# Performance work log

Hardware: AMD Instinct MI355X
Metric: run time of the kernel (lower is better)

## Reference

```python
import jax, jax.numpy as jnp
import numpy as np

# QLoRA NF4 levels (sorted), standard 16-value normal-float-4 codebook
NF4_LEVELS = jnp.array([
    -1.0, -0.6961928009986877, -0.5250730514526367, -0.39491748809814453,
    -0.28444138169288635, -0.18477343022823334, -0.09105003625154495, 0.0,
    0.07958029955625534, 0.16093020141124725, 0.24611230194568634,
    0.33791524171829224, 0.44070982933044434, 0.5626170039176941,
    0.8481764793395996, 1.0], dtype=jnp.float32)
NF4_MIDPOINTS = (NF4_LEVELS[1:] + NF4_LEVELS[:-1]) * 0.5  # nearest-level boundaries

BLOCK_SIZE = 64
SIGMA_FACTOR = 3.0
EPS = 1e-12


def fake_quantize_tcfp12(x, block_size=BLOCK_SIZE, nf4_residual=True,
                         nf_aware_scaling=True, sigma_factor=SIGMA_FACTOR):
    """Block-wise TCFP-12 fake quantize: int8 main component (nf-aware scale)
    + NF4-quantized residual. Returns dequantized tensor, same shape as x."""
    shape = x.shape
    xb = x.reshape(-1, block_size)                      # [N, B]
    absmax = jnp.max(jnp.abs(xb), axis=1, keepdims=True)
    if nf_aware_scaling:
        std = jnp.std(xb, axis=1, keepdims=True)
        scale = jnp.minimum(absmax, sigma_factor * std)
    else:
        scale = absmax
    scale = jnp.maximum(scale, EPS)
    # 8-bit symmetric main quantize (values beyond scale are clipped)
    q = jnp.clip(jnp.round(xb / scale * 127.0), -127.0, 127.0)
    main = q * (scale / 127.0)
    # 4-bit NF4 residual
    res = xb - main
    if nf4_residual:
        rmax = jnp.maximum(jnp.max(jnp.abs(res), axis=1, keepdims=True), EPS)
        rn = res / rmax                                  # normalized to [-1, 1]
        idx = jnp.searchsorted(NF4_MIDPOINTS, rn)        # nearest NF4 level
        rq = NF4_LEVELS[idx] * rmax
    else:
        rmax = jnp.maximum(jnp.max(jnp.abs(res), axis=1, keepdims=True), EPS)
        rq = jnp.clip(jnp.round(res / rmax * 7.0), -7.0, 7.0) * (rmax / 7.0)
    return (main + rq).reshape(shape)


def ste_fake_quantize(x):
    # straight-through estimator: forward quantizes, backward is identity
    return x + jax.lax.stop_gradient(fake_quantize_tcfp12(x) - x)


def setup_inputs() -> dict:
    key = jax.random.key(0)
    k1, k2 = jax.random.split(key)
    num_embeddings, embedding_dim = 50257, 768
    batch, seq = 8, 4096
    indices = jax.random.randint(k1, (batch, seq), 0, num_embeddings, dtype=jnp.int64 if jax.config.jax_enable_x64 else jnp.int32)
    weight = jax.random.normal(k2, (num_embeddings, embedding_dim), dtype=jnp.float32)
    weight = weight.at[0].set(0.0)  # padding_idx = 0
    return {"indices": indices, "weight": weight}


def reference(indices, weight):
    raw = weight[indices]            # [batch, seq, embedding_dim] gather
    return ste_fake_quantize(raw)
```

## Files before the change

### kernel.cpp

```cpp
#include <hip/hip_runtime.h>
#include <cstddef>


typedef float fx4 __attribute__((ext_vector_type(4)));
typedef int   ix2 __attribute__((ext_vector_type(2)));

namespace {

constexpr float kL[16] = {
    -1.0f, -0.6961928009986877f, -0.5250730514526367f, -0.39491748809814453f,
    -0.28444138169288635f, -0.18477343022823334f, -0.09105003625154495f, 0.0f,
    0.07958029955625534f, 0.16093020141124725f, 0.24611230194568634f,
    0.33791524171829224f, 0.44070982933044434f, 0.5626170039176941f,
    0.8481764793395996f, 1.0f};

}

__device__ __constant__ float kNF4Levels[16] = {
    -1.0f, -0.6961928009986877f, -0.5250730514526367f, -0.39491748809814453f,
    -0.28444138169288635f, -0.18477343022823334f, -0.09105003625154495f, 0.0f,
    0.07958029955625534f, 0.16093020141124725f, 0.24611230194568634f,
    0.33791524171829224f, 0.44070982933044434f, 0.5626170039176941f,
    0.8481764793395996f, 1.0f};

template <int CTRL>
__device__ __forceinline__ float dpp_rorf(float v) {
  return __builtin_bit_cast(
      float, __builtin_amdgcn_update_dpp(0, __builtin_bit_cast(int, v), CTRL,
                                         0xF, 0xF, true));
}

__device__ __forceinline__ fx4 tcfp12_quantize(fx4 x, const ix2* bins) {
  float am = fmaxf(fmaxf(fabsf(x.x), fabsf(x.y)), fmaxf(fabsf(x.z), fabsf(x.w)));
  float s  = (x.x + x.y) + (x.z + x.w);
  float ss = fmaf(x.x, x.x, fmaf(x.y, x.y, fmaf(x.z, x.z, x.w * x.w)));
  am = fmaxf(am, dpp_rorf<0x121>(am)); s += dpp_rorf<0x121>(s); ss += dpp_rorf<0x121>(ss);
  am = fmaxf(am, dpp_rorf<0x122>(am)); s += dpp_rorf<0x122>(s); ss += dpp_rorf<0x122>(ss);
  am = fmaxf(am, dpp_rorf<0x124>(am)); s += dpp_rorf<0x124>(s); ss += dpp_rorf<0x124>(ss);
  am = fmaxf(am, dpp_rorf<0x128>(am)); s += dpp_rorf<0x128>(s); ss += dpp_rorf<0x128>(ss);

  const float mean  = s * 0.015625f;
  const float var   = fmaxf(ss * 0.015625f - mean * mean, 0.0f);
  const float scale = fmaxf(fminf(am, 3.0f * sqrtf(var)), 1e-12f);
  const float to_q   = 127.0f / scale;
  const float from_q = scale / 127.0f;

  const float q0 = __builtin_amdgcn_fmed3f(rintf(x.x * to_q), -127.0f, 127.0f);
  const float q1 = __builtin_amdgcn_fmed3f(rintf(x.y * to_q), -127.0f, 127.0f);
  const float q2 = __builtin_amdgcn_fmed3f(rintf(x.z * to_q), -127.0f, 127.0f);
  const float q3 = __builtin_amdgcn_fmed3f(rintf(x.w * to_q), -127.0f, 127.0f);
  const float m0 = q0 * from_q, m1 = q1 * from_q, m2 = q2 * from_q, m3 = q3 * from_q;
  const float r0 = x.x - m0, r1 = x.y - m1, r2 = x.z - m2, r3 = x.w - m3;

  float rm = fmaxf(fmaxf(fabsf(r0), fabsf(r1)), fmaxf(fabsf(r2), fabsf(r3)));
  rm = fmaxf(rm, dpp_rorf<0x121>(rm));
  rm = fmaxf(rm, dpp_rorf<0x122>(rm));
  rm = fmaxf(rm, dpp_rorf<0x124>(rm));
  rm = fmaxf(rm, dpp_rorf<0x128>(rm));
  rm = fmaxf(rm, 1e-12f);
  const float invr = 1.0f / rm;
  const float rmq  = rm * (1.0f / 127.0f);

  fx4 o;
#pragma unroll
  for (int e = 0; e < 4; ++e) {
    const float r  = (e == 0) ? r0 : (e == 1) ? r1 : (e == 2) ? r2 : r3;
    const float mn = (e == 0) ? m0 : (e == 1) ? m1 : (e == 2) ? m2 : m3;
    const float rn = r * invr;
    const float t  = fmaf(rn, 32.0f, 32.0f);
    int j = (int)t;
    j = (j > 63) ? 63 : j;
    const ix2 b = bins[j];
    const float mstar = __builtin_bit_cast(float, b.x);
    const int   off   = (rn > mstar) ? 8 : 0;
    const int   li    = (int)((signed char)((b.y >> off) & 0xff));
    const float oe = fmaf((float)li, rmq, mn);
    if (e == 0) o.x = oe; else if (e == 1) o.y = oe;
    else if (e == 2) o.z = oe; else o.w = oe;
  }
  return o;
}

__global__ void __launch_bounds__(192)
tcfp_embedding_kernel(const int* __restrict__ indices,
                      const float* __restrict__ weight,
                      float* __restrict__ out,
                      int dim, int nrows) {
  __shared__ ix2 bins[64];
  const int tid = threadIdx.x;
  if (tid < 64) {
    const int j = tid;
    const float L = j * 0.03125f - 1.0f;
    int base = 0;
#pragma unroll
    for (int k = 0; k < 15; ++k) {
      const float mid = (kL[k] + kL[k + 1]) * 0.5f;
      base += (mid < L) ? 1 : 0;
    }
    float mstar = 2.0f;
    float lo = kNF4Levels[base];
    float hi = lo;
    if (base < 15) {
      float mb = 0.0f;
#pragma unroll
      for (int k = 0; k < 15; ++k)
        if (k == base) mb = (kL[k] + kL[k + 1]) * 0.5f;
      if (mb < L + 0.03125f) {
        mstar = mb;
        hi = kNF4Levels[base + 1];
      }
    }
    const int lo_i = (int)rintf(lo * 127.0f);
    const int hi_i = (int)rintf(hi * 127.0f);
    ix2 b;
    b.x = __builtin_bit_cast(int, mstar);
    b.y = (lo_i & 0xff) | ((hi_i & 0xff) << 8);
    bins[j] = b;
  }
  __syncthreads();

  const int row0 = blockIdx.x * 2;
  const int row1 = row0 + 1;
  const int lane = tid & 63;
  const int col  = (tid >> 6) * 256 + lane * 4;
  const bool has1 = (row1 < nrows);

  const int w0 = indices[row0];
  const int w1 = has1 ? indices[row1] : w0;
  const fx4 x0 =
      *reinterpret_cast<const fx4*>(weight + (size_t)w0 * (size_t)dim + col);
  const fx4 x1 =
      *reinterpret_cast<const fx4*>(weight + (size_t)w1 * (size_t)dim + col);

  const fx4 o0 = tcfp12_quantize(x0, bins);
  const fx4 o1 = tcfp12_quantize(x1, bins);

  __builtin_nontemporal_store(
      o0, reinterpret_cast<fx4*>(out + (size_t)row0 * (size_t)dim + col));
  if (has1)
    __builtin_nontemporal_store(
        o1, reinterpret_cast<fx4*>(out + (size_t)row1 * (size_t)dim + col));
}

extern "C" void kernel_launch(void* const* d_in, const int* in_sizes, int n_in,
                              void* d_out, int out_size, void* d_ws, size_t ws_size,
                              hipStream_t stream) {
  const int*   indices = (const int*)d_in[0];
  const float* weight  = (const float*)d_in[1];
  float*       out     = (float*)d_out;

  const int nrows = in_sizes[0];
  const int dim   = out_size / nrows;
  const int threads = dim / 4;
  const int grid = (nrows + 1) / 2;

  tcfp_embedding_kernel<<<grid, threads, 0, stream>>>(indices, weight, out,
                                                      dim, nrows);
}
```

Measured before the change: 35.52 us.

## Add persistent wave-strided kernel with software-prefetched loads for dim 768

For dim 768, each wave of a fixed 2048-block grid now processes one 64-element strip at a time in a grid-stride loop. It prefetches the next strip's gathered row before quantizing and storing the current one. The aim is to amortize the bins-table setup and the block launch cost, and to overlap gather latency with compute. The trade-off is fewer resident loads in flight per wave than the old two-rows-per-block layout, and a fixed grid size that may not saturate memory bandwidth.

```diff
diff --git a/kernel.cpp b/kernel.cpp
--- a/kernel.cpp
+++ b/kernel.cpp
@@ -30,64 +30,7 @@
                                          0xF, 0xF, true));
 }
 
-__device__ __forceinline__ fx4 tcfp12_quantize(fx4 x, const ix2* bins) {
-  float am = fmaxf(fmaxf(fabsf(x.x), fabsf(x.y)), fmaxf(fabsf(x.z), fabsf(x.w)));
-  float s  = (x.x + x.y) + (x.z + x.w);
-  float ss = fmaf(x.x, x.x, fmaf(x.y, x.y, fmaf(x.z, x.z, x.w * x.w)));
-  am = fmaxf(am, dpp_rorf<0x121>(am)); s += dpp_rorf<0x121>(s); ss += dpp_rorf<0x121>(ss);
-  am = fmaxf(am, dpp_rorf<0x122>(am)); s += dpp_rorf<0x122>(s); ss += dpp_rorf<0x122>(ss);
-  am = fmaxf(am, dpp_rorf<0x124>(am)); s += dpp_rorf<0x124>(s); ss += dpp_rorf<0x124>(ss);
-  am = fmaxf(am, dpp_rorf<0x128>(am)); s += dpp_rorf<0x128>(s); ss += dpp_rorf<0x128>(ss);
-
-  const float mean  = s * 0.015625f;
-  const float var   = fmaxf(ss * 0.015625f - mean * mean, 0.0f);
-  const float scale = fmaxf(fminf(am, 3.0f * sqrtf(var)), 1e-12f);
-  const float to_q   = 127.0f / scale;
-  const float from_q = scale / 127.0f;
-
-  const float q0 = __builtin_amdgcn_fmed3f(rintf(x.x * to_q), -127.0f, 127.0f);
-  const float q1 = __builtin_amdgcn_fmed3f(rintf(x.y * to_q), -127.0f, 127.0f);
-  const float q2 = __builtin_amdgcn_fmed3f(rintf(x.z * to_q), -127.0f, 127.0f);
-  const float q3 = __builtin_amdgcn_fmed3f(rintf(x.w * to_q), -127.0f, 127.0f);
-  const float m0 = q0 * from_q, m1 = q1 * from_q, m2 = q2 * from_q, m3 = q3 * from_q;
-  const float r0 = x.x - m0, r1 = x.y - m1, r2 = x.z - m2, r3 = x.w - m3;
-
-  float rm = fmaxf(fmaxf(fabsf(r0), fabsf(r1)), fmaxf(fabsf(r2), fabsf(r3)));
-  rm = fmaxf(rm, dpp_rorf<0x121>(rm));
-  rm = fmaxf(rm, dpp_rorf<0x122>(rm));
-  rm = fmaxf(rm, dpp_rorf<0x124>(rm));
-  rm = fmaxf(rm, dpp_rorf<0x128>(rm));
-  rm = fmaxf(rm, 1e-12f);
-  const float invr = 1.0f / rm;
-  const float rmq  = rm * (1.0f / 127.0f);
-
-  fx4 o;
-#pragma unroll
-  for (int e = 0; e < 4; ++e) {
-    const float r  = (e == 0) ? r0 : (e == 1) ? r1 : (e == 2) ? r2 : r3;
-    const float mn = (e == 0) ? m0 : (e == 1) ? m1 : (e == 2) ? m2 : m3;
-    const float rn = r * invr;
-    const float t  = fmaf(rn, 32.0f, 32.0f);
-    int j = (int)t;
-    j = (j > 63) ? 63 : j;
-    const ix2 b = bins[j];
-    const float mstar = __builtin_bit_cast(float, b.x);
-    const int   off   = (rn > mstar) ? 8 : 0;
-    const int   li    = (int)((signed char)((b.y >> off) & 0xff));
-    const float oe = fmaf((float)li, rmq, mn);
-    if (e == 0) o.x = oe; else if (e == 1) o.y = oe;
-    else if (e == 2) o.z = oe; else o.w = oe;
-  }
-  return o;
-}
-
-__global__ void __launch_bounds__(192)
-tcfp_embedding_kernel(const int* __restrict__ indices,
-                      const float* __restrict__ weight,
-                      float* __restrict__ out,
-                      int dim, int nrows) {
-  __shared__ ix2 bins[64];
-  const int tid = threadIdx.x;
+__device__ __forceinline__ void build_bins(ix2* bins, int tid) {
   if (tid < 64) {
     const int j = tid;
     const float L = j * 0.03125f - 1.0f;
@@ -117,6 +60,108 @@
     b.y = (lo_i & 0xff) | ((hi_i & 0xff) << 8);
     bins[j] = b;
   }
+}
+
+__device__ __forceinline__ fx4 tcfp12_quantize(fx4 x, const ix2* bins) {
+  float am = fmaxf(fmaxf(fabsf(x.x), fabsf(x.y)), fmaxf(fabsf(x.z), fabsf(x.w)));
+  float s  = (x.x + x.y) + (x.z + x.w);
+  float ss = fmaf(x.x, x.x, fmaf(x.y, x.y, fmaf(x.z, x.z, x.w * x.w)));
+  am = fmaxf(am, dpp_rorf<0x121>(am)); s += dpp_rorf<0x121>(s); ss += dpp_rorf<0x121>(ss);
+  am = fmaxf(am, dpp_rorf<0x122>(am)); s += dpp_rorf<0x122>(s); ss += dpp_rorf<0x122>(ss);
+  am = fmaxf(am, dpp_rorf<0x124>(am)); s += dpp_rorf<0x124>(s); ss += dpp_rorf<0x124>(ss);
+  am = fmaxf(am, dpp_rorf<0x128>(am)); s += dpp_rorf<0x128>(s); ss += dpp_rorf<0x128>(ss);
+
+  const float mean  = s * 0.015625f;
+  const float var   = fmaxf(ss * 0.015625f - mean * mean, 0.0f);
+  const float scale = fmaxf(fminf(am, 3.0f * sqrtf(var)), 1e-12f);
+  const float to_q   = 127.0f / scale;
+  const float from_q = scale / 127.0f;
+
+  const float q0 = __builtin_amdgcn_fmed3f(rintf(x.x * to_q), -127.0f, 127.0f);
+  const float q1 = __builtin_amdgcn_fmed3f(rintf(x.y * to_q), -127.0f, 127.0f);
+  const float q2 = __builtin_amdgcn_fmed3f(rintf(x.z * to_q), -127.0f, 127.0f);
+  const float q3 = __builtin_amdgcn_fmed3f(rintf(x.w * to_q), -127.0f, 127.0f);
+  const float m0 = q0 * from_q, m1 = q1 * from_q, m2 = q2 * from_q, m3 = q3 * from_q;
+  const float r0 = x.x - m0, r1 = x.y - m1, r2 = x.z - m2, r3 = x.w - m3;
+
+  float rm = fmaxf(fmaxf(fabsf(r0), fabsf(r1)), fmaxf(fabsf(r2), fabsf(r3)));
+  rm = fmaxf(rm, dpp_rorf<0x121>(rm));
+  rm = fmaxf(rm, dpp_rorf<0x122>(rm));
+  rm = fmaxf(rm, dpp_rorf<0x124>(rm));
+  rm = fmaxf(rm, dpp_rorf<0x128>(rm));
+  rm = fmaxf(rm, 1e-12f);
+  const float invr = 1.0f / rm;
+  const float rmq  = rm * (1.0f / 127.0f);
+
+  fx4 o;
+#pragma unroll
+  for (int e = 0; e < 4; ++e) {
+    const float r  = (e == 0) ? r0 : (e == 1) ? r1 : (e == 2) ? r2 : r3;
+    const float mn = (e == 0) ? m0 : (e == 1) ? m1 : (e == 2) ? m2 : m3;
+    const float rn = r * invr;
+    const float t  = fmaf(rn, 32.0f, 32.0f);
+    int j = (int)t;
+    j = (j > 63) ? 63 : j;
+    const ix2 b = bins[j];
+    const float mstar = __builtin_bit_cast(float, b.x);
+    const int   off   = (rn > mstar) ? 8 : 0;
+    const int   li    = (int)((signed char)((b.y >> off) & 0xff));
+    const float oe = fmaf((float)li, rmq, mn);
+    if (e == 0) o.x = oe; else if (e == 1) o.y = oe;
+    else if (e == 2) o.z = oe; else o.w = oe;
+  }
+  return o;
+}
+
+__global__ void __launch_bounds__(256)
+tcfp_embedding_768_persist(const int* __restrict__ indices,
+                           const float* __restrict__ weight,
+                           float* __restrict__ out,
+                           int nstrips, int wave_stride) {
+  __shared__ ix2 bins[64];
+  const int tid = threadIdx.x;
+  build_bins(bins, tid);
+  __syncthreads();
+
+  const int lane    = tid & 63;
+  const int col_off = lane * 4;
+  int s = __builtin_amdgcn_readfirstlane(blockIdx.x * 4 + (tid >> 6));
+  if (s >= nstrips) return;
+
+  int row = s / 3;
+  int col = (s - row * 3) * 256 + col_off;
+  fx4 x = *reinterpret_cast<const fx4*>(
+      weight + (size_t)indices[row] * 768 + col);
+  size_t ooff = (size_t)row * 768 + col;
+
+  for (;;) {
+    const int s_next = s + wave_stride;
+    const bool more  = s_next < nstrips;
+    fx4 xn;
+    size_t ooff_n = 0;
+    if (more) {
+      const int rn = s_next / 3;
+      const int cn = (s_next - rn * 3) * 256 + col_off;
+      xn = *reinterpret_cast<const fx4*>(
+          weight + (size_t)indices[rn] * 768 + cn);
+      ooff_n = (size_t)rn * 768 + cn;
+    }
+
+    const fx4 o = tcfp12_quantize(x, bins);
+    __builtin_nontemporal_store(o, reinterpret_cast<fx4*>(out + ooff));
+
+    if (!more) break;
+    x = xn; ooff = ooff_n; s = s_next;
+  }
+}
+
+__global__ void tcfp_embedding_generic(const int* __restrict__ indices,
+                                       const float* __restrict__ weight,
+                                       float* __restrict__ out,
+                                       int dim, int nrows) {
+  __shared__ ix2 bins[64];
+  const int tid = threadIdx.x;
+  build_bins(bins, tid);
   __syncthreads();
 
   const int row0 = blockIdx.x * 2;
@@ -151,9 +196,18 @@
 
   const int nrows = in_sizes[0];
   const int dim   = out_size / nrows;
-  const int threads = dim / 4;
-  const int grid = (nrows + 1) / 2;
-
-  tcfp_embedding_kernel<<<grid, threads, 0, stream>>>(indices, weight, out,
-                                                      dim, nrows);
-}
+
+  if (dim == 768) {
+    const int nstrips = nrows * 3;
+    int grid = 2048;
+    if (grid * 4 > nstrips) grid = (nstrips + 3) / 4;
+    const int wave_stride = grid * 4;
+    tcfp_embedding_768_persist<<<grid, 256, 0, stream>>>(indices, weight, out,
+                                                         nstrips, wave_stride);
+  } else {
+    const int threads = dim / 4;
+    const int grid = (nrows + 1) / 2;
+    tcfp_embedding_generic<<<grid, threads, 0, stream>>>(indices, weight, out,
+                                                         dim, nrows);
+  }
+}
```

Result: slower. 39.12 us (+10.1%).
